# Kernel tuning notes

Measured on AMD Instinct MI355X. Metric: run time of the kernel, lower is better.

## Reference

```python
import jax, jax.numpy as jnp
import numpy as np

B, S, H, D = 1, 2048, 16, 128
CAUSAL = True


def setup_inputs() -> dict:
    key = jax.random.key(0)
    kq, kk, kv = jax.random.split(key, 3)
    query = jax.random.normal(kq, (B, S, H, D), dtype=jnp.float32)
    k_ = jax.random.normal(kk, (B, S, H, D), dtype=jnp.float32)
    v_ = jax.random.normal(kv, (B, S, H, D), dtype=jnp.float32)
    return {"query": query, "key": k_, "value": v_}


def reference(query, key, value):
    # Single-device equivalent of LongContextAttention:
    # Ulysses all-to-all and ring pass are identity on one rank; the math is
    # standard scaled-dot-product attention with flash-attn's default scale
    # softmax_scale = 1/sqrt(head_dim) and causal masking.
    d = query.shape[-1]
    scale = 1.0 / jnp.sqrt(jnp.asarray(d, dtype=query.dtype))
    # [B,S,H,D] x [B,T,H,D] -> [B,H,S,T]
    scores = jnp.einsum("bshd,bthd->bhst", query, key) * scale
    if CAUSAL:
        s, t = scores.shape[-2], scores.shape[-1]
        mask = jnp.tril(jnp.ones((s, t), dtype=bool))
        scores = jnp.where(mask, scores, jnp.finfo(scores.dtype).min)
    probs = jax.nn.softmax(scores, axis=-1)
    out = jnp.einsum("bhst,bthd->bshd", probs, value)
    return out
```

## Files before the change

### kernel.cpp

```cpp
#include <hip/hip_runtime.h>
#include <hip/hip_bf16.h>
#include <math.h>

#define SS 2048
#define HH 16
#define DD 128
#define HD (HH*DD)
#define QB 128
#define KVB 64

typedef __attribute__((ext_vector_type(8))) short bf16x8;
typedef __attribute__((ext_vector_type(16))) float f32x16;

__device__ __forceinline__ ushort f2bf(float f) {
  __hip_bfloat16 h = __float2bfloat16(f);
  return __builtin_bit_cast(ushort, h);
}
__device__ __forceinline__ uint pk2(float a, float b) {
  return ((uint)f2bf(b) << 16) | (uint)f2bf(a);
}
__device__ __forceinline__ float bf2f(ushort u) {
  uint x = ((uint)u) << 16;
  return __builtin_bit_cast(float, x);
}

__global__ __launch_bounds__(256, 2)
void attn_fwd(const float* __restrict__ Q, const float* __restrict__ K,
              const float* __restrict__ V,
              ushort* __restrict__ PO, float* __restrict__ PM,
              float* __restrict__ PL) {
  __shared__ alignas(16) ushort Klds[KVB * DD];
  __shared__ alignas(16) ushort VTlds[DD * KVB];

  const int tid  = threadIdx.x;
  const int lane = tid & 63;
  const int wid  = tid >> 6;
  const int q32  = lane & 31;
  const int hi   = lane >> 5;
  const int swz  = (q32 & 7) << 4;

  const int g2   = (tid >> 4) & 3;
  const int n16  = tid & 15;
  const int dstg = wid * 16 + n16;

  const int bx   = blockIdx.x;
  const int h    = bx & 15;
  const int rest = bx >> 4;
  const int pp   = rest >> 2;
  const int jj   = rest & 3;
  const int LA   = 2 * pp + 2;
  const int BND[5] = {0, 8, 17, 25, 34};
  const int tl = BND[jj], th = BND[jj + 1];

  const float SCALE = 1.44269504088896f / sqrtf((float)DD);
  const float* Kb = K + (size_t)h * DD;
  const float* Vb = V + (size_t)h * DD;

  uint4 kreg[4];
  uint2 vreg[2][4];

  for (int phase = 0; phase < 2; ++phase) {
    int qt, lo, hiT;
    if (phase == 0) { qt = pp;      lo = tl;               hiT = min(th, LA); }
    else            { qt = 15 - pp; lo = max(tl, LA) - LA; hiT = th - LA; }
    if (lo >= hiT) continue;

    const int qb = qt * QB;
    const int qw = qb + 32 * wid;
    const int qg = qw + q32;

    bf16x8 qf[8];
    {
      const float* qr = Q + ((size_t)qg * HH + h) * DD;
      #pragma unroll
      for (int ks = 0; ks < 8; ++ks) {
        float4 x = *(const float4*)&qr[16 * ks + 8 * hi];
        float4 y = *(const float4*)&qr[16 * ks + 8 * hi + 4];
        uint4 u;
        u.x = pk2(x.x * SCALE, x.y * SCALE);
        u.y = pk2(x.z * SCALE, x.w * SCALE);
        u.z = pk2(y.x * SCALE, y.y * SCALE);
        u.w = pk2(y.z * SCALE, y.w * SCALE);
        qf[ks] = __builtin_bit_cast(bf16x8, u);
      }
    }

    f32x16 acc[4];
    #pragma unroll
    for (int dt = 0; dt < 4; ++dt)
      #pragma unroll
      for (int e = 0; e < 16; ++e) acc[dt][e] = 0.f;
    float m = -1e30f, l = 0.f;

    {
      const int t0 = lo * KVB;
      #pragma unroll
      for (int it = 0; it < 4; ++it) {
        int e = tid + it * 256;
        int row = e >> 4, col = (e & 15) * 8;
        const float* src = &Kb[(size_t)(t0 + row) * HD + col];
        float4 a = *(const float4*)src;
        float4 b = *(const float4*)(src + 4);
        kreg[it].x = pk2(a.x, a.y); kreg[it].y = pk2(a.z, a.w);
        kreg[it].z = pk2(b.x, b.y); kreg[it].w = pk2(b.z, b.w);
      }
      #pragma unroll
      for (int half = 0; half < 2; ++half) {
        const int d = dstg + 64 * half;
        #pragma unroll
        for (int jv = 0; jv < 4; ++jv) {
          const int tt = 16 * jv + 4 * g2;
          const float* vp = &Vb[(size_t)(t0 + tt) * HD + d];
          vreg[half][jv].x = pk2(vp[0],      vp[HD]);
          vreg[half][jv].y = pk2(vp[2 * HD], vp[3 * HD]);
        }
      }
    }

    for (int itile = lo; itile < hiT; ++itile) {
      __syncthreads();
      #pragma unroll
      for (int it = 0; it < 4; ++it) {
        int e = tid + it * 256;
        int row = e >> 4;
        *(uint4*)((char*)Klds + ((e * 16) ^ ((row & 7) << 4))) = kreg[it];
      }
      #pragma unroll
      for (int half = 0; half < 2; ++half) {
        const int d = dstg + 64 * half;
        #pragma unroll
        for (int jv = 0; jv < 4; ++jv) {
          const int tt = 16 * jv + 4 * g2;
          *(uint2*)((char*)VTlds + ((d * 128 + tt * 2) ^ ((d & 7) << 4))) = vreg[half][jv];
        }
      }
      __syncthreads();

      if (itile + 1 < hiT) {
        const int t0n = (itile + 1) * KVB;
        #pragma unroll
        for (int it = 0; it < 4; ++it) {
          int e = tid + it * 256;
          int row = e >> 4, col = (e & 15) * 8;
          const float* src = &Kb[(size_t)(t0n + row) * HD + col];
          float4 a = *(const float4*)src;
          float4 b = *(const float4*)(src + 4);
          kreg[it].x = pk2(a.x, a.y); kreg[it].y = pk2(a.z, a.w);
          kreg[it].z = pk2(b.x, b.y); kreg[it].w = pk2(b.z, b.w);
        }
        #pragma unroll
        for (int half = 0; half < 2; ++half) {
          const int d = dstg + 64 * half;
          #pragma unroll
          for (int jv = 0; jv < 4; ++jv) {
            const int tt = 16 * jv + 4 * g2;
            const float* vp = &Vb[(size_t)(t0n + tt) * HD + d];
            vreg[half][jv].x = pk2(vp[0],      vp[HD]);
            vreg[half][jv].y = pk2(vp[2 * HD], vp[3 * HD]);
          }
        }
      }

      const int t0 = itile * KVB;

      f32x16 s0, s1;
      #pragma unroll
      for (int e = 0; e < 16; ++e) { s0[e] = 0.f; s1[e] = 0.f; }
      __builtin_amdgcn_s_setprio(1);
      #pragma unroll
      for (int ks = 0; ks < 8; ++ks) {
        bf16x8 a0 = *(const bf16x8*)((const char*)Klds +
                      ((q32 * 256 + 32 * ks + 16 * hi) ^ swz));
        s0 = __builtin_amdgcn_mfma_f32_32x32x16_bf16(a0, qf[ks], s0, 0, 0, 0);
      }
      #pragma unroll
      for (int ks = 0; ks < 8; ++ks) {
        bf16x8 a1 = *(const bf16x8*)((const char*)Klds +
                      (((q32 + 32) * 256 + 32 * ks + 16 * hi) ^ swz));
        s1 = __builtin_amdgcn_mfma_f32_32x32x16_bf16(a1, qf[ks], s1, 0, 0, 0);
      }
      __builtin_amdgcn_s_setprio(0);

      if (t0 + KVB - 1 > qw) {
        #pragma unroll
        for (int e = 0; e < 16; ++e) {
          int tloc = (e & 3) + 8 * (e >> 2) + 4 * hi;
          if (t0 + tloc > qg)      s0[e] = -INFINITY;
          if (t0 + 32 + tloc > qg) s1[e] = -INFINITY;
        }
      }

      float mr = -1e30f;
      #pragma unroll
      for (int e = 0; e < 16; ++e) mr = fmaxf(mr, fmaxf(s0[e], s1[e]));
      mr = fmaxf(mr, __shfl_xor(mr, 32));
      float mn = fmaxf(m, mr);
      float corr = exp2f(m - mn);
      m = mn;
      float ps = 0.f;
      #pragma unroll
      for (int e = 0; e < 16; ++e) {
        float p0 = exp2f(s0[e] - m); s0[e] = p0; ps += p0;
        float p1 = exp2f(s1[e] - m); s1[e] = p1; ps += p1;
      }
      ps += __shfl_xor(ps, 32);
      l = l * corr + ps;
      #pragma unroll
      for (int dt = 0; dt < 4; ++dt)
        #pragma unroll
        for (int e = 0; e < 16; ++e) acc[dt][e] *= corr;

      uint4 paf[4];
      #pragma unroll
      for (int tk = 0; tk < 4; ++tk) {
        float p0,p1,p2,p3,p4,p5,p6,p7;
        if (tk == 0) { p0=s0[0];p1=s0[1];p2=s0[2];p3=s0[3];p4=s0[4];p5=s0[5];p6=s0[6];p7=s0[7]; }
        else if (tk == 1) { p0=s0[8];p1=s0[9];p2=s0[10];p3=s0[11];p4=s0[12];p5=s0[13];p6=s0[14];p7=s0[15]; }
        else if (tk == 2) { p0=s1[0];p1=s1[1];p2=s1[2];p3=s1[3];p4=s1[4];p5=s1[5];p6=s1[6];p7=s1[7]; }
        else { p0=s1[8];p1=s1[9];p2=s1[10];p3=s1[11];p4=s1[12];p5=s1[13];p6=s1[14];p7=s1[15]; }
        uint A0 = pk2(p0, p1), A1 = pk2(p2, p3);
        uint B0 = pk2(p4, p5), B1 = pk2(p6, p7);
        uint x0 = hi ? A0 : B0, x1 = hi ? A1 : B1;
        uint r0 = (uint)__shfl_xor((int)x0, 32);
        uint r1 = (uint)__shfl_xor((int)x1, 32);
        paf[tk].x = hi ? r0 : A0;
        paf[tk].y = hi ? r1 : A1;
        paf[tk].z = hi ? B0 : r0;
        paf[tk].w = hi ? B1 : r1;
      }

      __builtin_amdgcn_s_setprio(1);
      #pragma unroll
      for (int dt = 0; dt < 4; ++dt) {
        #pragma unroll
        for (int tk = 0; tk < 4; ++tk) {
          bf16x8 va = *(const bf16x8*)((const char*)VTlds +
                        (((dt * 32 + q32) * 128 + 32 * tk + 16 * hi) ^ swz));
          bf16x8 pb = __builtin_bit_cast(bf16x8, paf[tk]);
          acc[dt] = __builtin_amdgcn_mfma_f32_32x32x16_bf16(va, pb, acc[dt], 0, 0, 0);
        }
      }
      __builtin_amdgcn_s_setprio(0);
    }

    const int slot = (((h * 8 + pp) * 4 + jj) * 2) + phase;
    ushort* po = PO + (size_t)slot * (QB * DD);
    const int row = 32 * wid + q32;
    #pragma unroll
    for (int dt = 0; dt < 4; ++dt) {
      #pragma unroll
      for (int rq = 0; rq < 4; ++rq) {
        int d = 32 * dt + 8 * rq + 4 * hi;
        uint2 w;
        w.x = pk2(acc[dt][4 * rq + 0], acc[dt][4 * rq + 1]);
        w.y = pk2(acc[dt][4 * rq + 2], acc[dt][4 * rq + 3]);
        *(uint2*)&po[row * DD + d] = w;
      }
    }
    if (hi == 0) {
      PM[(size_t)slot * QB + row] = m;
      PL[(size_t)slot * QB + row] = l;
    }
  }
}

__global__ __launch_bounds__(256, 4)
void attn_merge(const ushort* __restrict__ PO, const float* __restrict__ PM,
                const float* __restrict__ PL, float* __restrict__ O) {
  const int bx  = blockIdx.x;
  const int h   = bx & 15;
  const int qt  = bx >> 4;
  const int tid = threadIdx.x;
  const int r   = tid >> 1;
  const int dh  = (tid & 1) * 64;

  const int BND[5] = {0, 8, 17, 25, 34};
  const int pp    = (qt < 8) ? qt : (15 - qt);
  const int phase = (qt < 8) ? 0 : 1;
  const int LA    = 2 * pp + 2;

  float mv[4], lv[4];
  float M = -1e30f;
  #pragma unroll
  for (int jj = 0; jj < 4; ++jj) {
    bool inc = (phase == 0) ? (BND[jj] < LA) : (BND[jj + 1] > LA);
    int slot = (((h * 8 + pp) * 4 + jj) * 2) + phase;
    mv[jj] = inc ? PM[(size_t)slot * QB + r] : -1e30f;
    lv[jj] = inc ? PL[(size_t)slot * QB + r] : 0.f;
    M = fmaxf(M, mv[jj]);
  }
  float L = 0.f;
  float o[64];
  #pragma unroll
  for (int k2 = 0; k2 < 64; ++k2) o[k2] = 0.f;
  #pragma unroll
  for (int jj = 0; jj < 4; ++jj) {
    bool inc = (phase == 0) ? (BND[jj] < LA) : (BND[jj + 1] > LA);
    if (!inc) continue;
    int slot = (((h * 8 + pp) * 4 + jj) * 2) + phase;
    float w = exp2f(mv[jj] - M);
    L += lv[jj] * w;
    const ushort* src = PO + (size_t)slot * (QB * DD) + r * DD + dh;
    #pragma unroll
    for (int k4 = 0; k4 < 16; ++k4) {
      ushort4 u = *(const ushort4*)&src[4 * k4];
      o[4*k4+0] += bf2f(u.x) * w;
      o[4*k4+1] += bf2f(u.y) * w;
      o[4*k4+2] += bf2f(u.z) * w;
      o[4*k4+3] += bf2f(u.w) * w;
    }
  }
  float inv = 1.0f / L;
  float* op = O + ((size_t)(qt * QB + r) * HH + h) * DD + dh;
  #pragma unroll
  for (int k4 = 0; k4 < 16; ++k4) {
    float4 x = make_float4(o[4*k4]*inv, o[4*k4+1]*inv, o[4*k4+2]*inv, o[4*k4+3]*inv);
    *(float4*)&op[4 * k4] = x;
  }
}

extern "C" void kernel_launch(void* const* d_in, const int* in_sizes, int n_in,
                              void* d_out, int out_size, void* d_ws, size_t ws_size,
                              hipStream_t stream) {
  const float* Q = (const float*)d_in[0];
  const float* K = (const float*)d_in[1];
  const float* V = (const float*)d_in[2];
  float* O = (float*)d_out;

  const size_t po_elems = (size_t)1024 * QB * DD;
  ushort* PO = (ushort*)d_ws;
  float*  PM = (float*)(PO + po_elems);
  float*  PL = PM + (size_t)1024 * QB;

  attn_fwd<<<dim3(512), 256, 0, stream>>>(Q, K, V, PO, PM, PL);
  attn_merge<<<dim3(256), 256, 0, stream>>>(PO, PM, PL, O);
}
```

Measured before the change: 69.80 us.

## Double-buffer K/V tiles in LDS and add lazy softmax rescaling

Adds a second LDS buffer for K and V^T so the next tile is staged into the alternate buffer after the PV MFMAs. This removes one of the two block barriers per iteration. The online softmax now skips the max update and accumulator rescale when no row's max rises by more than 8 (log2 units) across the wavefront. The max and sum reductions are restructured as trees for more ILP. LDS usage doubles, which can hurt occupancy at 2 blocks/CU, and the lazy rescale allows unnormalized values up to 2^8.

```diff
diff --git a/kernel.cpp b/kernel.cpp
--- a/kernel.cpp
+++ b/kernel.cpp
@@ -29,8 +29,8 @@
               const float* __restrict__ V,
               ushort* __restrict__ PO, float* __restrict__ PM,
               float* __restrict__ PL) {
-  __shared__ alignas(16) ushort Klds[KVB * DD];
-  __shared__ alignas(16) ushort VTlds[DD * KVB];
+  __shared__ alignas(16) ushort Klds[2][KVB * DD];
+  __shared__ alignas(16) ushort VTlds[2][DD * KVB];
 
   const int tid  = threadIdx.x;
   const int lane = tid & 63;
@@ -58,6 +58,47 @@
 
   uint4 kreg[4];
   uint2 vreg[2][4];
+
+  auto loadt = [&](int t0) {
+    #pragma unroll
+    for (int it = 0; it < 4; ++it) {
+      int e = tid + it * 256;
+      int row = e >> 4, col = (e & 15) * 8;
+      const float* src = &Kb[(size_t)(t0 + row) * HD + col];
+      float4 a = *(const float4*)src;
+      float4 b = *(const float4*)(src + 4);
+      kreg[it].x = pk2(a.x, a.y); kreg[it].y = pk2(a.z, a.w);
+      kreg[it].z = pk2(b.x, b.y); kreg[it].w = pk2(b.z, b.w);
+    }
+    #pragma unroll
+    for (int half = 0; half < 2; ++half) {
+      const int d = dstg + 64 * half;
+      #pragma unroll
+      for (int jv = 0; jv < 4; ++jv) {
+        const int tt = 16 * jv + 4 * g2;
+        const float* vp = &Vb[(size_t)(t0 + tt) * HD + d];
+        vreg[half][jv].x = pk2(vp[0],      vp[HD]);
+        vreg[half][jv].y = pk2(vp[2 * HD], vp[3 * HD]);
+      }
+    }
+  };
+  auto staget = [&](int b) {
+    #pragma unroll
+    for (int it = 0; it < 4; ++it) {
+      int e = tid + it * 256;
+      int row = e >> 4;
+      *(uint4*)((char*)&Klds[b][0] + ((e * 16) ^ ((row & 7) << 4))) = kreg[it];
+    }
+    #pragma unroll
+    for (int half = 0; half < 2; ++half) {
+      const int d = dstg + 64 * half;
+      #pragma unroll
+      for (int jv = 0; jv < 4; ++jv) {
+        const int tt = 16 * jv + 4 * g2;
+        *(uint2*)((char*)&VTlds[b][0] + ((d * 128 + tt * 2) ^ ((d & 7) << 4))) = vreg[half][jv];
+      }
+    }
+  };
 
   for (int phase = 0; phase < 2; ++phase) {
     int qt, lo, hiT;
@@ -92,76 +133,19 @@
       for (int e = 0; e < 16; ++e) acc[dt][e] = 0.f;
     float m = -1e30f, l = 0.f;
 
-    {
-      const int t0 = lo * KVB;
-      #pragma unroll
-      for (int it = 0; it < 4; ++it) {
-        int e = tid + it * 256;
-        int row = e >> 4, col = (e & 15) * 8;
-        const float* src = &Kb[(size_t)(t0 + row) * HD + col];
-        float4 a = *(const float4*)src;
-        float4 b = *(const float4*)(src + 4);
-        kreg[it].x = pk2(a.x, a.y); kreg[it].y = pk2(a.z, a.w);
-        kreg[it].z = pk2(b.x, b.y); kreg[it].w = pk2(b.z, b.w);
-      }
-      #pragma unroll
-      for (int half = 0; half < 2; ++half) {
-        const int d = dstg + 64 * half;
-        #pragma unroll
-        for (int jv = 0; jv < 4; ++jv) {
-          const int tt = 16 * jv + 4 * g2;
-          const float* vp = &Vb[(size_t)(t0 + tt) * HD + d];
-          vreg[half][jv].x = pk2(vp[0],      vp[HD]);
-          vreg[half][jv].y = pk2(vp[2 * HD], vp[3 * HD]);
-        }
-      }
-    }
+    loadt(lo * KVB);
+    __syncthreads();
+    staget(0);
+    int cur = 0;
 
     for (int itile = lo; itile < hiT; ++itile) {
       __syncthreads();
-      #pragma unroll
-      for (int it = 0; it < 4; ++it) {
-        int e = tid + it * 256;
-        int row = e >> 4;
-        *(uint4*)((char*)Klds + ((e * 16) ^ ((row & 7) << 4))) = kreg[it];
-      }
-      #pragma unroll
-      for (int half = 0; half < 2; ++half) {
-        const int d = dstg + 64 * half;
-        #pragma unroll
-        for (int jv = 0; jv < 4; ++jv) {
-          const int tt = 16 * jv + 4 * g2;
-          *(uint2*)((char*)VTlds + ((d * 128 + tt * 2) ^ ((d & 7) << 4))) = vreg[half][jv];
-        }
-      }
-      __syncthreads();
-
-      if (itile + 1 < hiT) {
-        const int t0n = (itile + 1) * KVB;
-        #pragma unroll
-        for (int it = 0; it < 4; ++it) {
-          int e = tid + it * 256;
-          int row = e >> 4, col = (e & 15) * 8;
-          const float* src = &Kb[(size_t)(t0n + row) * HD + col];
-          float4 a = *(const float4*)src;
-          float4 b = *(const float4*)(src + 4);
-          kreg[it].x = pk2(a.x, a.y); kreg[it].y = pk2(a.z, a.w);
-          kreg[it].z = pk2(b.x, b.y); kreg[it].w = pk2(b.z, b.w);
-        }
-        #pragma unroll
-        for (int half = 0; half < 2; ++half) {
-          const int d = dstg + 64 * half;
-          #pragma unroll
-          for (int jv = 0; jv < 4; ++jv) {
-            const int tt = 16 * jv + 4 * g2;
-            const float* vp = &Vb[(size_t)(t0n + tt) * HD + d];
-            vreg[half][jv].x = pk2(vp[0],      vp[HD]);
-            vreg[half][jv].y = pk2(vp[2 * HD], vp[3 * HD]);
-          }
-        }
-      }
+      const bool more = (itile + 1 < hiT);
+      if (more) loadt((itile + 1) * KVB);
 
       const int t0 = itile * KVB;
+      const char* Kc = (const char*)&Klds[cur][0];
+      const char* Vc = (const char*)&VTlds[cur][0];
 
       f32x16 s0, s1;
       #pragma unroll
@@ -169,14 +153,12 @@
       __builtin_amdgcn_s_setprio(1);
       #pragma unroll
       for (int ks = 0; ks < 8; ++ks) {
-        bf16x8 a0 = *(const bf16x8*)((const char*)Klds +
-                      ((q32 * 256 + 32 * ks + 16 * hi) ^ swz));
+        bf16x8 a0 = *(const bf16x8*)(Kc + ((q32 * 256 + 32 * ks + 16 * hi) ^ swz));
         s0 = __builtin_amdgcn_mfma_f32_32x32x16_bf16(a0, qf[ks], s0, 0, 0, 0);
       }
       #pragma unroll
       for (int ks = 0; ks < 8; ++ks) {
-        bf16x8 a1 = *(const bf16x8*)((const char*)Klds +
-                      (((q32 + 32) * 256 + 32 * ks + 16 * hi) ^ swz));
+        bf16x8 a1 = *(const bf16x8*)(Kc + (((q32 + 32) * 256 + 32 * ks + 16 * hi) ^ swz));
         s1 = __builtin_amdgcn_mfma_f32_32x32x16_bf16(a1, qf[ks], s1, 0, 0, 0);
       }
       __builtin_amdgcn_s_setprio(0);
@@ -190,25 +172,42 @@
         }
       }
 
-      float mr = -1e30f;
-      #pragma unroll
-      for (int e = 0; e < 16; ++e) mr = fmaxf(mr, fmaxf(s0[e], s1[e]));
-      mr = fmaxf(mr, __shfl_xor(mr, 32));
-      float mn = fmaxf(m, mr);
-      float corr = exp2f(m - mn);
-      m = mn;
-      float ps = 0.f;
+      float tmx[8];
+      #pragma unroll
+      for (int e = 0; e < 8; ++e)
+        tmx[e] = fmaxf(fmaxf(s0[e], s0[e + 8]), fmaxf(s1[e], s1[e + 8]));
+      #pragma unroll
+      for (int st = 4; st >= 1; st >>= 1)
+        #pragma unroll
+        for (int e = 0; e < st; ++e) tmx[e] = fmaxf(tmx[e], tmx[e + st]);
+      float mr = fmaxf(tmx[0], __shfl_xor(tmx[0], 32));
+
+      if (!__all(mr <= m + 8.0f)) {
+        float mn = fmaxf(m, mr);
+        float corr = exp2f(m - mn);
+        m = mn;
+        l *= corr;
+        #pragma unroll
+        for (int dt = 0; dt < 4; ++dt)
+          #pragma unroll
+          for (int e = 0; e < 16; ++e) acc[dt][e] *= corr;
+      }
+
+      float ts[8];
+      #pragma unroll
+      for (int e = 0; e < 8; ++e) ts[e] = 0.f;
       #pragma unroll
       for (int e = 0; e < 16; ++e) {
-        float p0 = exp2f(s0[e] - m); s0[e] = p0; ps += p0;
-        float p1 = exp2f(s1[e] - m); s1[e] = p1; ps += p1;
-      }
-      ps += __shfl_xor(ps, 32);
-      l = l * corr + ps;
-      #pragma unroll
-      for (int dt = 0; dt < 4; ++dt)
-        #pragma unroll
-        for (int e = 0; e < 16; ++e) acc[dt][e] *= corr;
+        float p0 = exp2f(s0[e] - m); s0[e] = p0;
+        float p1 = exp2f(s1[e] - m); s1[e] = p1;
+        ts[e & 7] += p0 + p1;
+      }
+      #pragma unroll
+      for (int st = 4; st >= 1; st >>= 1)
+        #pragma unroll
+        for (int e = 0; e < st; ++e) ts[e] += ts[e + st];
+      float ps = ts[0] + __shfl_xor(ts[0], 32);
+      l += ps;
 
       uint4 paf[4];
       #pragma unroll
@@ -234,13 +233,16 @@
       for (int dt = 0; dt < 4; ++dt) {
         #pragma unroll
         for (int tk = 0; tk < 4; ++tk) {
-          bf16x8 va = *(const bf16x8*)((const char*)VTlds +
+          bf16x8 va = *(const bf16x8*)(Vc +
                         (((dt * 32 + q32) * 128 + 32 * tk + 16 * hi) ^ swz));
           bf16x8 pb = __builtin_bit_cast(bf16x8, paf[tk]);
           acc[dt] = __builtin_amdgcn_mfma_f32_32x32x16_bf16(va, pb, acc[dt], 0, 0, 0);
         }
       }
       __builtin_amdgcn_s_setprio(0);
+
+      if (more) staget(cur ^ 1);
+      cur ^= 1;
     }
 
     const int slot = (((h * 8 + pp) * 4 + jj) * 2) + phase;
```

Measured after the change: 65.04 us. 6.8% less time.
